# Kernel optimization log

Hardware: AMD Instinct MI355X
Metric: run time of the kernel (lower is better)

Reference implementation:

```python
import jax, jax.numpy as jnp
import jax.scipy.linalg
import numpy as np
import math

IMG = 512
PATCH = 14
NDIM = 2
HEAD_DIM = 128  # dim // heads = 4096 // 32
STEPS = math.ceil(IMG / PATCH)  # 37


def setup_inputs() -> dict:
    key = jax.random.key(0)
    k1, = jax.random.split(key, 1)
    gen = jax.random.uniform(k1, (NDIM, 1, HEAD_DIM, HEAD_DIM), dtype=jnp.float32) * (2.0 * math.pi)
    image_sizes = jnp.full((1, NDIM), IMG, dtype=jnp.int32)
    return {"image_sizes": image_sizes, "generator_raw_params": gen}


def _positions():
    # cartesian product of linspace(0,1,STEPS) along each axis -> [1, STEPS**NDIM, NDIM]
    axes = [jnp.linspace(0.0, 1.0, STEPS, dtype=jnp.float32) for _ in range(NDIM)]
    grid = jnp.stack(jnp.meshgrid(*axes, indexing="ij"), axis=-1).reshape(-1, NDIM)
    return grid[None]  # [1, N, NDIM]


def reference(image_sizes, generator_raw_params):
    positions = _positions()  # [1, N, NDIM]; image size is static (512) per jit requirements
    upper = jnp.triu(generator_raw_params, k=1) - 0.5  # [NDIM,1,D,D]
    skew = upper - jnp.swapaxes(upper, -1, -2)          # skew-symmetric bases
    # sum over input dims: generator per position, [1, N, 1, D, D]
    gen_pos = jnp.einsum("bnd,dhij->bnhij", positions, skew)
    cls = jnp.zeros_like(gen_pos[:, :1])                # CLS token generator (identity rotation)
    gen_pos = jnp.concatenate([cls, gen_pos], axis=1)   # [1, N+1, 1, D, D]
    b, n, h, d, _ = gen_pos.shape
    flat = gen_pos.astype(jnp.float32).reshape(b * n * h, d, d)
    rot = jax.vmap(jax.scipy.linalg.expm)(flat)
    return rot.reshape(b, n, h, d, d).astype(positions.dtype)
```

## Files before the change

### kernel.cpp

```cpp
#include <hip/hip_runtime.h>
#include <math.h>

#define STEPS 37
#define NMAT  (STEPS*STEPS + 1)
#define D     128
#define NT    1024

typedef _Float16 half8 __attribute__((ext_vector_type(8)));
typedef __fp16   fp16x2 __attribute__((ext_vector_type(2)));
typedef float    f32x4 __attribute__((ext_vector_type(4)));

#define PH_OFF   0
#define PL_OFF   32768
#define QTH_OFF  65536
#define QTL_OFF  98304
#define RED_OFF  131072
#define LDS_BYTES (131072 + 640)

__constant__ float dC[8] = {
    1.0f, 1.0f, 5.0e-1f, 1.6666666666666666e-1f, 4.1666666666666664e-2f,
    8.3333333333333332e-3f, 1.3888888888888889e-3f, 1.9841269841269841e-4f };

__device__ __forceinline__ int swzA(int r, int slot) {
    return r*256 + ((slot ^ (r & 7)) << 4);
}
__device__ __forceinline__ int swzE(int r, int c) {
    return r*256 + (((c >> 3) ^ (r & 7)) << 4) + ((c & 7) << 1);
}

template<bool WQT, bool WXR, bool WGL>
__device__ __forceinline__ void matmul_step(unsigned char* sm, float diagc,
                                            float* __restrict__ gout,
                                            int wr, int wc, int lr, int g)
{
    f32x4 acc1[2][2] = {};
    f32x4 acc2[2][2] = {};

    #pragma unroll
    for (int ks = 0; ks < 4; ++ks) {
        const int slot = 4*ks + g;
        half8 ah[2], al[2];
        #pragma unroll
        for (int bi = 0; bi < 2; ++bi) {
            const int r = wr*32 + bi*16 + lr;
            const int off = swzA(r, slot);
            ah[bi] = *(const half8*)(sm + PH_OFF + off);
            al[bi] = *(const half8*)(sm + PL_OFF + off);
        }
        #pragma unroll
        for (int bj = 0; bj < 2; ++bj) {
            const int c = wc*32 + bj*16 + lr;
            const int off = swzA(c, slot);
            const half8 qh = *(const half8*)(sm + QTH_OFF + off);
            const half8 ql = *(const half8*)(sm + QTL_OFF + off);
            #pragma unroll
            for (int bi = 0; bi < 2; ++bi) {
                acc1[bi][bj] = __builtin_amdgcn_mfma_f32_16x16x32_f16(ah[bi], qh, acc1[bi][bj], 0, 0, 0);
                acc2[bi][bj] = __builtin_amdgcn_mfma_f32_16x16x32_f16(ah[bi], ql, acc2[bi][bj], 0, 0, 0);
                acc2[bi][bj] = __builtin_amdgcn_mfma_f32_16x16x32_f16(al[bi], qh, acc2[bi][bj], 0, 0, 0);
            }
        }
    }

    if (WGL) {
        #pragma unroll
        for (int bi = 0; bi < 2; ++bi)
            #pragma unroll
            for (int bj = 0; bj < 2; ++bj) {
                const int col = wc*32 + bj*16 + lr;
                const int r0  = wr*32 + bi*16 + 4*g;
                #pragma unroll
                for (int q = 0; q < 4; ++q)
                    gout[(r0+q)*D + col] = acc1[bi][bj][q] + acc2[bi][bj][q] * (1.0f/2048.0f);
            }
        return;
    }

    uint2 uhv[2][2], ulv[2][2];
    #pragma unroll
    for (int bi = 0; bi < 2; ++bi) {
        #pragma unroll
        for (int bj = 0; bj < 2; ++bj) {
            const int col = wc*32 + bj*16 + lr;
            const int r0  = wr*32 + bi*16 + 4*g;
            float v[4];
            #pragma unroll
            for (int q = 0; q < 4; ++q)
                v[q] = acc1[bi][bj][q] + acc2[bi][bj][q] * (1.0f/2048.0f);
            if (wr*32 + bi*16 == wc*32 + bj*16) {
                #pragma unroll
                for (int q = 0; q < 4; ++q)
                    if (r0 + q == col) v[q] += diagc;
            }
            const fp16x2 h01 = __builtin_amdgcn_cvt_pkrtz(v[0], v[1]);
            const fp16x2 h23 = __builtin_amdgcn_cvt_pkrtz(v[2], v[3]);
            const fp16x2 l01 = __builtin_amdgcn_cvt_pkrtz((v[0]-(float)h01[0])*2048.f,
                                                          (v[1]-(float)h01[1])*2048.f);
            const fp16x2 l23 = __builtin_amdgcn_cvt_pkrtz((v[2]-(float)h23[0])*2048.f,
                                                          (v[3]-(float)h23[1])*2048.f);
            union { fp16x2 h2[2]; uint2 u; } cvh, cvl;
            cvh.h2[0] = h01; cvh.h2[1] = h23;
            cvl.h2[0] = l01; cvl.h2[1] = l23;
            uhv[bi][bj] = cvh.u; ulv[bi][bj] = cvl.u;
        }
    }
    __syncthreads();

    #pragma unroll
    for (int bi = 0; bi < 2; ++bi) {
        #pragma unroll
        for (int bj = 0; bj < 2; ++bj) {
            const int col = wc*32 + bj*16 + lr;
            const int r0  = wr*32 + bi*16 + 4*g;
            if (WQT) {
                const int off = col*256 + (((r0 >> 3) ^ (col & 7)) << 4) + ((g & 1) << 3);
                *(uint2*)(sm + QTH_OFF + off) = uhv[bi][bj];
                *(uint2*)(sm + QTL_OFF + off) = ulv[bi][bj];
            }
            if (WXR) {
                union { uint2 u; _Float16 h[4]; } th, tl;
                th.u = uhv[bi][bj]; tl.u = ulv[bi][bj];
                #pragma unroll
                for (int q = 0; q < 4; ++q) {
                    const int rr = r0 + q;
                    const int off = swzE(rr, col);
                    *(_Float16*)(sm + PH_OFF + off) = th.h[q];
                    *(_Float16*)(sm + PL_OFF + off) = tl.h[q];
                }
            }
        }
    }
    __syncthreads();
}

__global__ __launch_bounds__(NT)
void liere_expm_mfma(const float* __restrict__ gen, float* __restrict__ out)
{
    __shared__ __align__(16) unsigned char sm[LDS_BYTES];
    const int tid = threadIdx.x;
    const int wg  = blockIdx.x;

    float px = 0.f, py = 0.f;
    if (wg > 0) {
        const int idx = wg - 1;
        px = (float)(idx / STEPS) * (1.0f/(STEPS-1));
        py = (float)(idx % STEPS) * (1.0f/(STEPS-1));
    }

    float* Gp = (float*)sm;
    const float* g0 = gen;
    const float* g1 = gen + D*D;
    #pragma unroll
    for (int it = 0; it < 16; ++it) {
        const int e = tid + (it << 10);
        const int i = e >> 7, j = e & 127;
        if (i < j) {
            const float v = px*g0[e] + py*g1[e];
            Gp[i*132 + j] =  v;
            Gp[j*132 + i] = -v;
        } else if (i == j) {
            Gp[i*132 + j] = 0.f;
        }
    }
    __syncthreads();

    float* red = (float*)(sm + RED_OFF);
    if (tid < D) {
        float s = 0.f;
        const f32x4* rowp = (const f32x4*)&Gp[tid*132];
        #pragma unroll 8
        for (int u = 0; u < 32; ++u) {
            const f32x4 v = rowp[u];
            s += fabsf(v.x) + fabsf(v.y) + fabsf(v.z) + fabsf(v.w);
        }
        red[tid] = s;
    }
    __syncthreads();
    #pragma unroll
    for (int off = 64; off >= 1; off >>= 1) {
        if (tid < off) red[tid] = fmaxf(red[tid], red[tid + off]);
        __syncthreads();
    }
    const float m = red[0];
    int nsq = 0;
    if (m > 0.5f) nsq = (int)ceilf(log2f(m * 2.0f));
    if (nsq < 0) nsq = 0;
    const float scale = exp2f(-(float)nsq);

    float vst[16];
    #pragma unroll
    for (int it = 0; it < 16; ++it) {
        const int e = tid + (it << 10);
        vst[it] = Gp[(e>>7)*132 + (e&127)];
    }
    __syncthreads();

    {
        const float c7 = dC[7], c6 = dC[6];
        #pragma unroll
        for (int it = 0; it < 16; ++it) {
            const int e = tid + (it << 10);
            const int i = e >> 7, j = e & 127;
            const float p = vst[it] * scale;
            const _Float16 ph = (_Float16)p;
            const _Float16 pl = (_Float16)((p - (float)ph) * 2048.f);
            const int offP = swzE(i, j);
            *(_Float16*)(sm + PH_OFF + offP) = ph;
            *(_Float16*)(sm + PL_OFF + offP) = pl;
            const float x = c7*p + ((i == j) ? c6 : 0.f);
            const _Float16 xh = (_Float16)x;
            const _Float16 xl = (_Float16)((x - (float)xh) * 2048.f);
            const int offQ = swzE(j, i);
            *(_Float16*)(sm + QTH_OFF + offQ) = xh;
            *(_Float16*)(sm + QTL_OFF + offQ) = xl;
        }
    }
    __syncthreads();

    const int lid = tid & 63;
    const int wid = tid >> 6;
    const int wr = wid >> 2, wc = wid & 3;
    const int lr = lid & 15, g = lid >> 4;
    float* gout = out + (size_t)wg * (D*D);

    for (int kk = 5; kk >= 1; --kk)
        matmul_step<true, false, false>(sm, dC[kk], gout, wr, wc, lr, g);
    matmul_step<true, true, false>(sm, dC[0], gout, wr, wc, lr, g);

    if (nsq == 0) {
        #pragma unroll
        for (int it = 0; it < 16; ++it) {
            const int e = tid + (it << 10);
            const int i = e >> 7, j = e & 127;
            const int off = swzE(i, j);
            gout[e] = (float)*(_Float16*)(sm + PH_OFF + off)
                    + (float)*(_Float16*)(sm + PL_OFF + off) * (1.0f/2048.0f);
        }
        return;
    }

    for (int t = 0; t < nsq - 1; ++t)
        matmul_step<true, true, false>(sm, 0.f, gout, wr, wc, lr, g);
    matmul_step<false, false, true>(sm, 0.f, gout, wr, wc, lr, g);
}

extern "C" void kernel_launch(void* const* d_in, const int* in_sizes, int n_in,
                              void* d_out, int out_size, void* d_ws, size_t ws_size,
                              hipStream_t stream) {
    (void)in_sizes; (void)n_in; (void)d_ws; (void)ws_size; (void)out_size;
    const float* gen = (const float*)d_in[1];
    float* out = (float*)d_out;
    liere_expm_mfma<<<NMAT, NT, 0, stream>>>(gen, out);
}
```

Measured before the change: 457.0 us.

## Estimate spectral radius via power iteration to reduce squaring steps

Replaces the 1-norm-only choice of scaling-and-squaring count with a spectral estimate from six power iterations on two pseudo-random vectors. The count is clamped between the 1-norm bound minus three and the 1-norm bound, so fewer matrix squarings run per matrix. The max reduction also switches to wave shuffles instead of a log-step LDS loop with a barrier per step. The risk is lower accuracy, since the Taylor polynomial is now applied to matrices whose norm can exceed the previous bound, and the power iterations add extra barriers.

Result: slower. 489.1 us (+7.0%).

```diff
diff --git a/kernel.cpp b/kernel.cpp
--- a/kernel.cpp
+++ b/kernel.cpp
@@ -15,7 +15,9 @@
 #define QTH_OFF  65536
 #define QTL_OFF  98304
 #define RED_OFF  131072
-#define LDS_BYTES (131072 + 640)
+#define PIV_OFF  (131072 + 2048)
+#define SCAL_OFF (131072 + 4096)
+#define LDS_BYTES (131072 + 4096 + 64)
 
 __constant__ float dC[8] = {
     1.0f, 1.0f, 5.0e-1f, 1.6666666666666666e-1f, 4.1666666666666664e-2f,
@@ -164,7 +166,13 @@
     }
     __syncthreads();
 
-    float* red = (float*)(sm + RED_OFF);
+    float* red  = (float*)(sm + RED_OFF);
+    float* va   = (float*)(sm + PIV_OFF);
+    float* wa   = (float*)(sm + PIV_OFF + 512);
+    float* vb   = (float*)(sm + PIV_OFF + 1024);
+    float* wb   = (float*)(sm + PIV_OFF + 1536);
+    float* scal = (float*)(sm + SCAL_OFF);
+
     if (tid < D) {
         float s = 0.f;
         const f32x4* rowp = (const f32x4*)&Gp[tid*132];
@@ -174,17 +182,69 @@
             s += fabsf(v.x) + fabsf(v.y) + fabsf(v.z) + fabsf(v.w);
         }
         red[tid] = s;
-    }
-    __syncthreads();
-    #pragma unroll
-    for (int off = 64; off >= 1; off >>= 1) {
-        if (tid < off) red[tid] = fmaxf(red[tid], red[tid + off]);
-        __syncthreads();
-    }
-    const float m = red[0];
+        va[tid] = 0.5f + (float)((tid * 2654435761u) >> 24) * (1.0f/256.0f);
+        vb[tid] = 0.5f + (float)((tid * 1597334677u) >> 24) * (1.0f/256.0f);
+    }
+    __syncthreads();
+    if (tid < 64) {
+        float a = fmaxf(red[tid], red[tid + 64]);
+        a = fmaxf(a, __shfl_xor(a, 32)); a = fmaxf(a, __shfl_xor(a, 16));
+        a = fmaxf(a, __shfl_xor(a, 8));  a = fmaxf(a, __shfl_xor(a, 4));
+        a = fmaxf(a, __shfl_xor(a, 2));  a = fmaxf(a, __shfl_xor(a, 1));
+        if (tid == 0) scal[0] = a;
+    }
+    __syncthreads();
+
+    {
+        const int i = tid >> 3, p = tid & 7;
+        const float* row = &Gp[i*132 + p*16];
+        #pragma unroll
+        for (int itm = 0; itm < 6; ++itm) {
+            const float* sa = (itm & 1) ? wa : va;
+            const float* sb = (itm & 1) ? wb : vb;
+            float* da = (itm & 1) ? va : wa;
+            float* db = (itm & 1) ? vb : wb;
+            float pa = 0.f, pb = 0.f;
+            #pragma unroll
+            for (int u = 0; u < 16; ++u) {
+                const float gv = row[u];
+                pa += gv * sa[p*16 + u];
+                pb += gv * sb[p*16 + u];
+            }
+            pa += __shfl_xor(pa, 4); pa += __shfl_xor(pa, 2); pa += __shfl_xor(pa, 1);
+            pb += __shfl_xor(pb, 4); pb += __shfl_xor(pb, 2); pb += __shfl_xor(pb, 1);
+            if (p == 0) { da[i] = pa; db[i] = pb; }
+            __syncthreads();
+        }
+    }
+    if (tid < D) {
+        red[tid]       = wa[tid]*wa[tid];
+        red[128 + tid] = va[tid]*va[tid];
+        red[256 + tid] = wb[tid]*wb[tid];
+        red[384 + tid] = vb[tid]*vb[tid];
+    }
+    __syncthreads();
+    if (tid < 256) {
+        const int grp = tid >> 6, l = tid & 63;
+        float a = red[grp*128 + l] + red[grp*128 + l + 64];
+        a += __shfl_xor(a, 32); a += __shfl_xor(a, 16); a += __shfl_xor(a, 8);
+        a += __shfl_xor(a, 4);  a += __shfl_xor(a, 2);  a += __shfl_xor(a, 1);
+        if (l == 0) scal[1 + grp] = a;
+    }
+    __syncthreads();
+
+    const float m1  = scal[0];
+    const float n5a = scal[1], n6a = scal[2], n5b = scal[3], n6b = scal[4];
+    int s1 = 0;
+    if (m1 > 0.5f) { s1 = (int)ceilf(log2f(m1 * 2.0f)); if (s1 < 0) s1 = 0; }
+    const float sea = (n5a > 1e-20f) ? sqrtf(n6a / n5a) : 0.f;
+    const float seb = (n5b > 1e-20f) ? sqrtf(n6b / n5b) : 0.f;
+    const float sg  = fmaxf(sea, seb) * 1.25f;
     int nsq = 0;
-    if (m > 0.5f) nsq = (int)ceilf(log2f(m * 2.0f));
-    if (nsq < 0) nsq = 0;
+    if (sg > 0.5f) { nsq = (int)ceilf(log2f(sg * 2.0f)); if (nsq < 0) nsq = 0; }
+    int lo = s1 - 3; if (lo < 0) lo = 0;
+    if (nsq < lo) nsq = lo;
+    if (nsq > s1) nsq = s1;
     const float scale = exp2f(-(float)nsq);
 
     float vst[16];
```
